# Kernel optimization log

Measured on AMD Instinct MI355X. Metric: run time of the kernel, lower is better.

Reference implementation:

```python
import jax, jax.numpy as jnp
import numpy as np
from jax import lax

T, IMG, C_IN = 2048, 84, 4
HID = 256
NUM_OUT = 18
FEAT = 6 * 6 * 32  # 84 -> 42 -> 21 -> 11 -> 6 with stride-2 SAME convs


def setup_inputs() -> dict:
    key = jax.random.key(0)
    ks = jax.random.split(key, 8)
    d = {}
    d["x"] = jax.random.normal(ks[0], (T, IMG, IMG, C_IN), jnp.float32)
    cin = C_IN
    for i in range(4):
        d[f"conv_w{i}"] = jax.random.normal(ks[1 + i], (3, 3, cin, 32), jnp.float32) * (1.0 / np.sqrt(9 * cin))
        d[f"conv_b{i}"] = jnp.zeros((32,), jnp.float32)
        cin = 32
    d["lstm_w"] = jax.random.normal(ks[5], (FEAT + HID, 4 * HID), jnp.float32) * (1.0 / np.sqrt(FEAT + HID))
    d["lstm_b"] = jnp.zeros((4 * HID,), jnp.float32)
    d["fc_w"] = jax.random.normal(ks[6], (HID, NUM_OUT), jnp.float32) * 0.01
    d["fc_b"] = jnp.zeros((NUM_OUT,), jnp.float32)
    d["c_in"] = jnp.zeros((1, HID), jnp.float32)
    d["h_in"] = jnp.zeros((1, HID), jnp.float32)
    return d


def _conv_stack(x, ws, bs):
    dn = ("NHWC", "HWIO", "NHWC")
    for w, b in zip(ws, bs):
        x = jax.nn.elu(lax.conv_general_dilated(x, w, (2, 2), "SAME", dimension_numbers=dn) + b)
    return x.reshape(x.shape[0], -1)  # [T, FEAT]


def _lstm(feats, c0, h0, lstm_w, lstm_b):
    # BasicLSTMCell: gates [i, j, f, o], forget_bias = 1.0
    def step(carry, xt):
        c, h = carry  # [1, HID] each
        z = jnp.concatenate([xt[None, :], h], axis=1) @ lstm_w + lstm_b
        i, j, f, o = jnp.split(z, 4, axis=1)
        c = c * jax.nn.sigmoid(f + 1.0) + jax.nn.sigmoid(i) * jnp.tanh(j)
        h = jnp.tanh(c) * jax.nn.sigmoid(o)
        return (c, h), h[0]

    (_, _), hs = lax.scan(step, (c0, h0), feats)
    return hs  # [T, HID]


def reference(x, c_in, h_in,
              conv_w0, conv_b0, conv_w1, conv_b1,
              conv_w2, conv_b2, conv_w3, conv_b3,
              lstm_w, lstm_b, fc_w, fc_b):
    feats = _conv_stack(x, [conv_w0, conv_w1, conv_w2, conv_w3],
                        [conv_b0, conv_b1, conv_b2, conv_b3])
    hs = _lstm(feats, c_in, h_in, lstm_w, lstm_b)
    logits = hs @ fc_w + fc_b  # [T, NUM_OUT]
    return logits, hs
```

## Files before the change

### kernel.cpp

```cpp
#include <hip/hip_runtime.h>
#include <hip/hip_bf16.h>

__device__ inline float fsig(float x) { return 1.0f / (1.0f + __expf(-x)); }
__device__ inline float ftanh(float x) {
    float ax = fabsf(x);
    float e = __expf(-2.0f * ax);
    float r = (1.0f - e) / (1.0f + e);
    return x >= 0.0f ? r : -r;
}
__device__ inline float felu(float x) { return x > 0.0f ? x : expm1f(x); }

typedef _Float16 h2_t __attribute__((ext_vector_type(2)));
typedef _Float16 f16x8 __attribute__((ext_vector_type(8)));
typedef float f32x4 __attribute__((ext_vector_type(4)));

__device__ inline unsigned int packh2(float a, float b) {
    unsigned short ua = __builtin_bit_cast(unsigned short, (_Float16)a);
    unsigned short ub = __builtin_bit_cast(unsigned short, (_Float16)b);
    return (unsigned int)ua | ((unsigned int)ub << 16);
}
__device__ inline unsigned short f16bits(float a) {
    return __builtin_bit_cast(unsigned short, (_Float16)a);
}

__device__ inline float dot2acc(unsigned int w, unsigned int h, float acc) {
#if __has_builtin(__builtin_amdgcn_fdot2)
    return __builtin_amdgcn_fdot2(__builtin_bit_cast(h2_t, w), __builtin_bit_cast(h2_t, h), acc, false);
#else
    _Float16 wlo = __builtin_bit_cast(_Float16, (unsigned short)(w & 0xffff));
    _Float16 whi = __builtin_bit_cast(_Float16, (unsigned short)(w >> 16));
    _Float16 hlo = __builtin_bit_cast(_Float16, (unsigned short)(h & 0xffff));
    _Float16 hhi = __builtin_bit_cast(_Float16, (unsigned short)(h >> 16));
    return acc + (float)wlo * (float)hlo + (float)whi * (float)hhi;
#endif
}

__global__ __launch_bounds__(256) void convert_lwT(const float* __restrict__ lw,
                                                   unsigned short* __restrict__ lwhT) {
    int idx = blockIdx.x * 256 + threadIdx.x;
    if (idx >= 1152 * 1024) return;
    int k = idx >> 10, n = idx & 1023;
    lwhT[(size_t)n * 1152 + k] = f16bits(lw[idx]);
}

__global__ __launch_bounds__(256) void conv0_kernel(const float* __restrict__ in,
                                                    const float* __restrict__ wg,
                                                    const float* __restrict__ bias,
                                                    unsigned short* __restrict__ out) {
    constexpr int W = 84, OW = 42, PAD = 0, WP = W + 2;
    __shared__ float in_s[3 * WP * 4];
    constexpr int NQ = 3 * WP;
    const int tid = threadIdx.x;
    const int oy = blockIdx.x;
    const int t = blockIdx.y;
    const int co = tid & 31;

    for (int q = tid; q < NQ; q += 256) {
        int ky = q / WP;
        int col = q - ky * WP;
        int iy = 2 * oy - PAD + ky;
        int ix = col - 1;
        float4 v = make_float4(0.f, 0.f, 0.f, 0.f);
        if (iy >= 0 && iy < W && ix >= 0 && ix < W)
            v = *(const float4*)&in[(((size_t)t * W + iy) * W + ix) * 4];
        *(float4*)&in_s[q * 4] = v;
    }

    float wr[9][4];
#pragma unroll
    for (int tap = 0; tap < 9; ++tap)
#pragma unroll
        for (int j = 0; j < 4; ++j) wr[tap][j] = wg[(tap * 4 + j) * 32 + co];
    __syncthreads();

    const int g = tid >> 5;
    constexpr int NOX = (OW + 7) / 8;
    float acc[NOX];
#pragma unroll
    for (int m = 0; m < NOX; ++m) acc[m] = 0.f;
#pragma unroll
    for (int ky = 0; ky < 3; ++ky)
#pragma unroll
        for (int kx = 0; kx < 3; ++kx) {
            float w0 = wr[ky * 3 + kx][0], w1 = wr[ky * 3 + kx][1];
            float w2 = wr[ky * 3 + kx][2], w3 = wr[ky * 3 + kx][3];
#pragma unroll
            for (int m = 0; m < NOX; ++m) {
                int ox = g + 8 * m;
                if (ox < OW) {
                    int cs = 2 * ox + kx - PAD + 1;
                    float4 xi = *(const float4*)&in_s[(ky * WP + cs) * 4];
                    acc[m] += xi.x * w0 + xi.y * w1 + xi.z * w2 + xi.w * w3;
                }
            }
        }
    float b = bias[co];
#pragma unroll
    for (int m = 0; m < NOX; ++m) {
        int ox = g + 8 * m;
        if (ox < OW)
            out[(((size_t)t * OW + oy) * OW + ox) * 32 + co] = f16bits(felu(acc[m] + b));
    }
}

template <int W, int OW, int PAD, bool F32OUT>
__global__ __launch_bounds__(256) void convh_kernel(const unsigned short* __restrict__ in,
                                                    const float* __restrict__ wg,
                                                    const float* __restrict__ bias,
                                                    void* __restrict__ outv) {
    constexpr int WP = W + 2;
    constexpr int OWQ = (OW + 3) / 4;
    __shared__ __align__(16) unsigned short in_s[3][WP][32];
    __shared__ float zs[4][OW * 32];

    const int tid = threadIdx.x;
    const int oy = blockIdx.x;
    const int t = blockIdx.y;
    const int co16 = tid & 15;
    const int cig = (tid >> 4) & 3;
    const int oxq = tid >> 6;

    constexpr int NQ4 = 3 * WP * 4;
    uint4* in_s4 = reinterpret_cast<uint4*>(&in_s[0][0][0]);
    for (int q = tid; q < NQ4; q += 256) {
        int ky = q / (WP * 4);
        int rem = q - ky * (WP * 4);
        int col = rem >> 2, c4 = rem & 3;
        int iy = 2 * oy - PAD + ky;
        int ix = col - 1;
        uint4 v = make_uint4(0u, 0u, 0u, 0u);
        if (iy >= 0 && iy < W && ix >= 0 && ix < W)
            v = *(const uint4*)&in[(((size_t)t * W + iy) * W + ix) * 32 + c4 * 8];
        in_s4[q] = v;
    }

    unsigned int wr[9][4][2];
#pragma unroll
    for (int tap = 0; tap < 9; ++tap)
#pragma unroll
        for (int p = 0; p < 4; ++p) {
            wr[tap][p][0] = packh2(wg[(tap * 32 + cig * 8 + 2 * p) * 32 + co16],
                                   wg[(tap * 32 + cig * 8 + 2 * p + 1) * 32 + co16]);
            wr[tap][p][1] = packh2(wg[(tap * 32 + cig * 8 + 2 * p) * 32 + co16 + 16],
                                   wg[(tap * 32 + cig * 8 + 2 * p + 1) * 32 + co16 + 16]);
        }
    __syncthreads();

    float acc0[OWQ], acc1[OWQ];
#pragma unroll
    for (int m = 0; m < OWQ; ++m) { acc0[m] = 0.f; acc1[m] = 0.f; }
#pragma unroll
    for (int ky = 0; ky < 3; ++ky)
#pragma unroll
        for (int kx = 0; kx < 3; ++kx) {
            const int tap = ky * 3 + kx;
#pragma unroll
            for (int m = 0; m < OWQ; ++m) {
                int ox = oxq * OWQ + m;
                if (ox < OW) {
                    int cs = 2 * ox + kx - PAD + 1;
                    uint4 h8 = *(const uint4*)&in_s[ky][cs][cig * 8];
                    acc0[m] = dot2acc(wr[tap][0][0], h8.x, acc0[m]);
                    acc0[m] = dot2acc(wr[tap][1][0], h8.y, acc0[m]);
                    acc0[m] = dot2acc(wr[tap][2][0], h8.z, acc0[m]);
                    acc0[m] = dot2acc(wr[tap][3][0], h8.w, acc0[m]);
                    acc1[m] = dot2acc(wr[tap][0][1], h8.x, acc1[m]);
                    acc1[m] = dot2acc(wr[tap][1][1], h8.y, acc1[m]);
                    acc1[m] = dot2acc(wr[tap][2][1], h8.z, acc1[m]);
                    acc1[m] = dot2acc(wr[tap][3][1], h8.w, acc1[m]);
                }
            }
        }
#pragma unroll
    for (int m = 0; m < OWQ; ++m) {
        int ox = oxq * OWQ + m;
        if (ox < OW) {
            zs[cig][ox * 32 + co16] = acc0[m];
            zs[cig][ox * 32 + co16 + 16] = acc1[m];
        }
    }
    __syncthreads();

    for (int idx = tid; idx < OW * 32; idx += 256) {
        float s = zs[0][idx] + zs[1][idx] + zs[2][idx] + zs[3][idx] + bias[idx & 31];
        s = felu(s);
        if constexpr (F32OUT)
            ((float*)outv)[(((size_t)t * OW + oy) * OW) * 32 + idx] = s;
        else
            ((unsigned short*)outv)[(((size_t)t * OW + oy) * OW) * 32 + idx] = f16bits(s);
    }
}

__global__ __launch_bounds__(256) void gemm_mfma(const unsigned short* __restrict__ A,
                                                 const unsigned short* __restrict__ BT,
                                                 const float* __restrict__ bias,
                                                 float* __restrict__ C) {
    __shared__ __align__(16) unsigned short As[64][40];
    __shared__ __align__(16) unsigned short Bs[64][40];
    const int bn = blockIdx.x;
    const int bm = blockIdx.y;
    const int tid = threadIdx.x;
    const int wv = tid >> 6;
    const int l = tid & 63;
    const int lm = l & 15;
    const int kg = l >> 4;

    f32x4 acc[4] = {};

    const int sr = tid >> 2;
    const int sk = (tid & 3) * 8;

    for (int k0 = 0; k0 < 1152; k0 += 32) {
        *(uint4*)&As[sr][sk] = *(const uint4*)&A[(size_t)(bm * 64 + sr) * 1152 + k0 + sk];
        *(uint4*)&Bs[sr][sk] = *(const uint4*)&BT[(size_t)(bn * 64 + sr) * 1152 + k0 + sk];
        __syncthreads();

        f16x8 a = *(const f16x8*)&As[(wv << 4) + lm][kg * 8];
        f16x8 b0 = *(const f16x8*)&Bs[lm][kg * 8];
        f16x8 b1 = *(const f16x8*)&Bs[16 + lm][kg * 8];
        f16x8 b2 = *(const f16x8*)&Bs[32 + lm][kg * 8];
        f16x8 b3 = *(const f16x8*)&Bs[48 + lm][kg * 8];
        acc[0] = __builtin_amdgcn_mfma_f32_16x16x32_f16(a, b0, acc[0], 0, 0, 0);
        acc[1] = __builtin_amdgcn_mfma_f32_16x16x32_f16(a, b1, acc[1], 0, 0, 0);
        acc[2] = __builtin_amdgcn_mfma_f32_16x16x32_f16(a, b2, acc[2], 0, 0, 0);
        acc[3] = __builtin_amdgcn_mfma_f32_16x16x32_f16(a, b3, acc[3], 0, 0, 0);
        __syncthreads();
    }

#pragma unroll
    for (int nt = 0; nt < 4; ++nt) {
        int col = bn * 64 + nt * 16 + lm;
        float bv = bias[col];
#pragma unroll
        for (int j = 0; j < 4; ++j) {
            int row = bm * 64 + (wv << 4) + kg * 4 + j;
            C[(size_t)row * 1024 + col] = acc[nt][j] + bv;
        }
    }
}

__global__ __attribute__((amdgpu_flat_work_group_size(512, 512)))
void lstm7_kernel(const float* __restrict__ lstm_w,
                  const float* __restrict__ xpart,
                  const float* __restrict__ c_in,
                  const float* __restrict__ h_in,
                  float* __restrict__ hs_out) {
    __shared__ __align__(16) unsigned int wl[512][52];
    __shared__ float zsm[2][4][256];
    __shared__ __align__(16) unsigned int hpk[2][2][68];

    const int tid = threadIdx.x;
    const int s = tid >> 8;
    const int u = tid & 255;

    for (int q = 0; q < 4; ++q)
        for (int p = 0; p < 12; ++p) {
            int gp = 64 * s + p;
            wl[tid][q * 12 + p] = packh2(lstm_w[(size_t)(1152 + 2 * gp) * 1024 + (q << 8) + u],
                                         lstm_w[(size_t)(1152 + 2 * gp + 1) * 1024 + (q << 8) + u]);
        }
    unsigned int wreg[4][52];
#pragma unroll
    for (int q = 0; q < 4; ++q)
        for (int p = 12; p < 64; ++p) {
            int gp = 64 * s + p;
            wreg[q][p - 12] = packh2(lstm_w[(size_t)(1152 + 2 * gp) * 1024 + (q << 8) + u],
                                     lstm_w[(size_t)(1152 + 2 * gp + 1) * 1024 + (q << 8) + u]);
        }

    float c_state = c_in[u];
    if (tid < 256) {
        unsigned short* hrow = (unsigned short*)&hpk[0][u >> 7][0];
        hrow[u & 127] = f16bits(h_in[u]);
    }
    __syncthreads();

    float xp0 = xpart[u], xp1 = xpart[256 + u], xp2 = xpart[512 + u], xp3 = xpart[768 + u];

    for (int t = 0; t < 2048; ++t) {
        const int cur = t & 1;
        const uint4* hq = reinterpret_cast<const uint4*>(&hpk[cur][s][0]);

        float a0 = 0.f, a1 = 0.f, a2 = 0.f, a3 = 0.f;
        {
            uint4 hA = hq[0], hB = hq[1], hC = hq[2];
            uint4 w0a = *(const uint4*)&wl[tid][0];
            uint4 w0b = *(const uint4*)&wl[tid][4];
            uint4 w0c = *(const uint4*)&wl[tid][8];
            a0 = dot2acc(w0a.x, hA.x, a0); a0 = dot2acc(w0a.y, hA.y, a0);
            a0 = dot2acc(w0a.z, hA.z, a0); a0 = dot2acc(w0a.w, hA.w, a0);
            a0 = dot2acc(w0b.x, hB.x, a0); a0 = dot2acc(w0b.y, hB.y, a0);
            a0 = dot2acc(w0b.z, hB.z, a0); a0 = dot2acc(w0b.w, hB.w, a0);
            a0 = dot2acc(w0c.x, hC.x, a0); a0 = dot2acc(w0c.y, hC.y, a0);
            a0 = dot2acc(w0c.z, hC.z, a0); a0 = dot2acc(w0c.w, hC.w, a0);
            uint4 w1a = *(const uint4*)&wl[tid][12];
            uint4 w1b = *(const uint4*)&wl[tid][16];
            uint4 w1c = *(const uint4*)&wl[tid][20];
            a1 = dot2acc(w1a.x, hA.x, a1); a1 = dot2acc(w1a.y, hA.y, a1);
            a1 = dot2acc(w1a.z, hA.z, a1); a1 = dot2acc(w1a.w, hA.w, a1);
            a1 = dot2acc(w1b.x, hB.x, a1); a1 = dot2acc(w1b.y, hB.y, a1);
            a1 = dot2acc(w1b.z, hB.z, a1); a1 = dot2acc(w1b.w, hB.w, a1);
            a1 = dot2acc(w1c.x, hC.x, a1); a1 = dot2acc(w1c.y, hC.y, a1);
            a1 = dot2acc(w1c.z, hC.z, a1); a1 = dot2acc(w1c.w, hC.w, a1);
            uint4 w2a = *(const uint4*)&wl[tid][24];
            uint4 w2b = *(const uint4*)&wl[tid][28];
            uint4 w2c = *(const uint4*)&wl[tid][32];
            a2 = dot2acc(w2a.x, hA.x, a2); a2 = dot2acc(w2a.y, hA.y, a2);
            a2 = dot2acc(w2a.z, hA.z, a2); a2 = dot2acc(w2a.w, hA.w, a2);
            a2 = dot2acc(w2b.x, hB.x, a2); a2 = dot2acc(w2b.y, hB.y, a2);
            a2 = dot2acc(w2b.z, hB.z, a2); a2 = dot2acc(w2b.w, hB.w, a2);
            a2 = dot2acc(w2c.x, hC.x, a2); a2 = dot2acc(w2c.y, hC.y, a2);
            a2 = dot2acc(w2c.z, hC.z, a2); a2 = dot2acc(w2c.w, hC.w, a2);
            uint4 w3a = *(const uint4*)&wl[tid][36];
            uint4 w3b = *(const uint4*)&wl[tid][40];
            uint4 w3c = *(const uint4*)&wl[tid][44];
            a3 = dot2acc(w3a.x, hA.x, a3); a3 = dot2acc(w3a.y, hA.y, a3);
            a3 = dot2acc(w3a.z, hA.z, a3); a3 = dot2acc(w3a.w, hA.w, a3);
            a3 = dot2acc(w3b.x, hB.x, a3); a3 = dot2acc(w3b.y, hB.y, a3);
            a3 = dot2acc(w3b.z, hB.z, a3); a3 = dot2acc(w3b.w, hB.w, a3);
            a3 = dot2acc(w3c.x, hC.x, a3); a3 = dot2acc(w3c.y, hC.y, a3);
            a3 = dot2acc(w3c.z, hC.z, a3); a3 = dot2acc(w3c.w, hC.w, a3);
        }
#pragma unroll
        for (int c = 3; c < 16; ++c) {
            uint4 h4 = hq[c];
            const int r = 4 * (c - 3);
            a0 = dot2acc(wreg[0][r + 0], h4.x, a0); a0 = dot2acc(wreg[0][r + 1], h4.y, a0);
            a0 = dot2acc(wreg[0][r + 2], h4.z, a0); a0 = dot2acc(wreg[0][r + 3], h4.w, a0);
            a1 = dot2acc(wreg[1][r + 0], h4.x, a1); a1 = dot2acc(wreg[1][r + 1], h4.y, a1);
            a1 = dot2acc(wreg[1][r + 2], h4.z, a1); a1 = dot2acc(wreg[1][r + 3], h4.w, a1);
            a2 = dot2acc(wreg[2][r + 0], h4.x, a2); a2 = dot2acc(wreg[2][r + 1], h4.y, a2);
            a2 = dot2acc(wreg[2][r + 2], h4.z, a2); a2 = dot2acc(wreg[2][r + 3], h4.w, a2);
            a3 = dot2acc(wreg[3][r + 0], h4.x, a3); a3 = dot2acc(wreg[3][r + 1], h4.y, a3);
            a3 = dot2acc(wreg[3][r + 2], h4.z, a3); a3 = dot2acc(wreg[3][r + 3], h4.w, a3);
        }
        zsm[s][0][u] = a0;
        zsm[s][1][u] = a1;
        zsm[s][2][u] = a2;
        zsm[s][3][u] = a3;

        float xn0 = 0.f, xn1 = 0.f, xn2 = 0.f, xn3 = 0.f;
        if (t + 1 < 2048) {
            const float* xr = &xpart[(size_t)(t + 1) * 1024];
            xn0 = xr[u]; xn1 = xr[256 + u]; xn2 = xr[512 + u]; xn3 = xr[768 + u];
        }

        asm volatile("s_waitcnt lgkmcnt(0)\n\ts_barrier" ::: "memory");

        float zi = zsm[0][0][u] + zsm[1][0][u] + xp0;
        float zj = zsm[0][1][u] + zsm[1][1][u] + xp1;
        float zf = zsm[0][2][u] + zsm[1][2][u] + xp2;
        float zo = zsm[0][3][u] + zsm[1][3][u] + xp3;
        c_state = c_state * fsig(zf + 1.0f) + fsig(zi) * ftanh(zj);
        float h = ftanh(c_state) * fsig(zo);
        if (tid < 256) {
            hs_out[(size_t)t * 256 + u] = h;
            unsigned short* hrow = (unsigned short*)&hpk[cur ^ 1][u >> 7][0];
            hrow[u & 127] = f16bits(h);
        }

        asm volatile("s_waitcnt lgkmcnt(0)\n\ts_barrier" ::: "memory");
        xp0 = xn0; xp1 = xn1; xp2 = xn2; xp3 = xn3;
    }
}

__global__ void logits_kernel(const float* __restrict__ hs, const float* __restrict__ fc_w,
                              const float* __restrict__ fc_b, float* __restrict__ out) {
    int idx = blockIdx.x * 256 + threadIdx.x;
    if (idx >= 2048 * 18) return;
    int t = idx / 18, n = idx % 18;
    float acc = fc_b[n];
    const float* hrow = hs + (size_t)t * 256;
#pragma unroll 4
    for (int k = 0; k < 256; ++k) acc += hrow[k] * fc_w[k * 18 + n];
    out[idx] = acc;
}

extern "C" void kernel_launch(void* const* d_in, const int* in_sizes, int n_in,
                              void* d_out, int out_size, void* d_ws, size_t ws_size,
                              hipStream_t stream) {
    const float* x   = (const float*)d_in[0];
    const float* w0  = (const float*)d_in[1];
    const float* b0  = (const float*)d_in[2];
    const float* w1  = (const float*)d_in[3];
    const float* b1  = (const float*)d_in[4];
    const float* w2  = (const float*)d_in[5];
    const float* b2  = (const float*)d_in[6];
    const float* w3  = (const float*)d_in[7];
    const float* b3  = (const float*)d_in[8];
    const float* lw  = (const float*)d_in[9];
    const float* lb  = (const float*)d_in[10];
    const float* fcw = (const float*)d_in[11];
    const float* fcb = (const float*)d_in[12];
    const float* cin = (const float*)d_in[13];
    const float* hin = (const float*)d_in[14];

    float* outp = (float*)d_out;
    float* hs_out = outp + 2048 * 18;

    float* xpart = (float*)d_ws;
    unsigned short* feats16 = (unsigned short*)(xpart + (size_t)2048 * 1024);
    unsigned short* lwhT = feats16 + (size_t)2048 * 1152;
    unsigned short* bufs = lwhT + (size_t)1024 * 1152;

    const size_t FIXED_B = (size_t)2048 * 1024 * 4 + (size_t)2048 * 1152 * 2 +
                           (size_t)1024 * 1152 * 2;
    const size_t PERT_B = ((size_t)56448 + 14112 + 3872) * 2;

    int C = 128;
    const int cands[5] = {2048, 1024, 512, 256, 128};
    for (int i = 0; i < 5; ++i) {
        if (FIXED_B + (size_t)cands[i] * PERT_B <= ws_size) { C = cands[i]; break; }
    }

    unsigned short* c0buf = bufs;
    unsigned short* c1buf = c0buf + (size_t)C * 56448;
    unsigned short* c2buf = c1buf + (size_t)C * 14112;

    convert_lwT<<<4608, 256, 0, stream>>>(lw, lwhT);

    for (int t0 = 0; t0 < 2048; t0 += C) {
        const float* xin = x + (size_t)t0 * 84 * 84 * 4;
        conv0_kernel<<<dim3(42, C), 256, 0, stream>>>(xin, w0, b0, c0buf);
        convh_kernel<42, 21, 0, false><<<dim3(21, C), 256, 0, stream>>>(c0buf, w1, b1, c1buf);
        convh_kernel<21, 11, 1, false><<<dim3(11, C), 256, 0, stream>>>(c1buf, w2, b2, c2buf);
        convh_kernel<11, 6, 1, false><<<dim3(6, C), 256, 0, stream>>>(
            c2buf, w3, b3, feats16 + (size_t)t0 * 1152);
    }

    gemm_mfma<<<dim3(16, 32), 256, 0, stream>>>(feats16, lwhT, lb, xpart);
    lstm7_kernel<<<1, 512, 0, stream>>>(lw, xpart, cin, hin, hs_out);
    logits_kernel<<<144, 256, 0, stream>>>(hs_out, fcw, fcb, outp);
}
```

Baseline: 4.377 ms.

## Broadcast LSTM hidden state via readlane and tile the weight transpose

The recurrent LSTM step now has each lane load one 16-byte slice of the packed hidden state and broadcasts it across the wavefront with readlane. This replaces per-lane LDS reads of the whole h vector and cuts LDS traffic on the serial critical path. Gate math and the xpart prefetch are restricted to the 256 threads that own outputs, removing redundant work in the second half of the block. The fp16 weight transpose becomes a shared-memory tiled transpose so both global reads and writes are coalesced. The readlane sequence adds scalar-unit instructions and may raise register pressure.

```diff
diff --git a/kernel.cpp b/kernel.cpp
--- a/kernel.cpp
+++ b/kernel.cpp
@@ -37,10 +37,15 @@
 
 __global__ __launch_bounds__(256) void convert_lwT(const float* __restrict__ lw,
                                                    unsigned short* __restrict__ lwhT) {
-    int idx = blockIdx.x * 256 + threadIdx.x;
-    if (idx >= 1152 * 1024) return;
-    int k = idx >> 10, n = idx & 1023;
-    lwhT[(size_t)n * 1152 + k] = f16bits(lw[idx]);
+    __shared__ float tile[32][33];
+    const int kb = blockIdx.x * 32;
+    const int nb = blockIdx.y * 32;
+    const int tx = threadIdx.x & 31, ty = threadIdx.x >> 5;
+    for (int i = ty; i < 32; i += 8)
+        tile[i][tx] = lw[(size_t)(kb + i) * 1024 + nb + tx];
+    __syncthreads();
+    for (int i = ty; i < 32; i += 8)
+        lwhT[(size_t)(nb + i) * 1152 + kb + tx] = f16bits(tile[tx][i]);
 }
 
 __global__ __launch_bounds__(256) void conv0_kernel(const float* __restrict__ in,
@@ -240,11 +245,11 @@
 }
 
 __global__ __attribute__((amdgpu_flat_work_group_size(512, 512)))
-void lstm7_kernel(const float* __restrict__ lstm_w,
-                  const float* __restrict__ xpart,
-                  const float* __restrict__ c_in,
-                  const float* __restrict__ h_in,
-                  float* __restrict__ hs_out) {
+void lstm10_kernel(const float* __restrict__ lstm_w,
+                   const float* __restrict__ xpart,
+                   const float* __restrict__ c_in,
+                   const float* __restrict__ h_in,
+                   float* __restrict__ hs_out) {
     __shared__ __align__(16) unsigned int wl[512][52];
     __shared__ float zsm[2][4][256];
     __shared__ __align__(16) unsigned int hpk[2][2][68];
@@ -275,64 +280,45 @@
     }
     __syncthreads();
 
-    float xp0 = xpart[u], xp1 = xpart[256 + u], xp2 = xpart[512 + u], xp3 = xpart[768 + u];
+    float xp0 = 0.f, xp1 = 0.f, xp2 = 0.f, xp3 = 0.f;
+    if (tid < 256) {
+        xp0 = xpart[u]; xp1 = xpart[256 + u]; xp2 = xpart[512 + u]; xp3 = xpart[768 + u];
+    }
 
     for (int t = 0; t < 2048; ++t) {
         const int cur = t & 1;
-        const uint4* hq = reinterpret_cast<const uint4*>(&hpk[cur][s][0]);
+        uint4 hv = *(const uint4*)&hpk[cur][s][(tid & 15) * 4];
+
+        unsigned int wlo[4][12];
+#pragma unroll
+        for (int q = 0; q < 4; ++q) {
+            *(uint4*)&wlo[q][0] = *(const uint4*)&wl[tid][q * 12 + 0];
+            *(uint4*)&wlo[q][4] = *(const uint4*)&wl[tid][q * 12 + 4];
+            *(uint4*)&wlo[q][8] = *(const uint4*)&wl[tid][q * 12 + 8];
+        }
 
         float a0 = 0.f, a1 = 0.f, a2 = 0.f, a3 = 0.f;
-        {
-            uint4 hA = hq[0], hB = hq[1], hC = hq[2];
-            uint4 w0a = *(const uint4*)&wl[tid][0];
-            uint4 w0b = *(const uint4*)&wl[tid][4];
-            uint4 w0c = *(const uint4*)&wl[tid][8];
-            a0 = dot2acc(w0a.x, hA.x, a0); a0 = dot2acc(w0a.y, hA.y, a0);
-            a0 = dot2acc(w0a.z, hA.z, a0); a0 = dot2acc(w0a.w, hA.w, a0);
-            a0 = dot2acc(w0b.x, hB.x, a0); a0 = dot2acc(w0b.y, hB.y, a0);
-            a0 = dot2acc(w0b.z, hB.z, a0); a0 = dot2acc(w0b.w, hB.w, a0);
-            a0 = dot2acc(w0c.x, hC.x, a0); a0 = dot2acc(w0c.y, hC.y, a0);
-            a0 = dot2acc(w0c.z, hC.z, a0); a0 = dot2acc(w0c.w, hC.w, a0);
-            uint4 w1a = *(const uint4*)&wl[tid][12];
-            uint4 w1b = *(const uint4*)&wl[tid][16];
-            uint4 w1c = *(const uint4*)&wl[tid][20];
-            a1 = dot2acc(w1a.x, hA.x, a1); a1 = dot2acc(w1a.y, hA.y, a1);
-            a1 = dot2acc(w1a.z, hA.z, a1); a1 = dot2acc(w1a.w, hA.w, a1);
-            a1 = dot2acc(w1b.x, hB.x, a1); a1 = dot2acc(w1b.y, hB.y, a1);
-            a1 = dot2acc(w1b.z, hB.z, a1); a1 = dot2acc(w1b.w, hB.w, a1);
-            a1 = dot2acc(w1c.x, hC.x, a1); a1 = dot2acc(w1c.y, hC.y, a1);
-            a1 = dot2acc(w1c.z, hC.z, a1); a1 = dot2acc(w1c.w, hC.w, a1);
-            uint4 w2a = *(const uint4*)&wl[tid][24];
-            uint4 w2b = *(const uint4*)&wl[tid][28];
-            uint4 w2c = *(const uint4*)&wl[tid][32];
-            a2 = dot2acc(w2a.x, hA.x, a2); a2 = dot2acc(w2a.y, hA.y, a2);
-            a2 = dot2acc(w2a.z, hA.z, a2); a2 = dot2acc(w2a.w, hA.w, a2);
-            a2 = dot2acc(w2b.x, hB.x, a2); a2 = dot2acc(w2b.y, hB.y, a2);
-            a2 = dot2acc(w2b.z, hB.z, a2); a2 = dot2acc(w2b.w, hB.w, a2);
-            a2 = dot2acc(w2c.x, hC.x, a2); a2 = dot2acc(w2c.y, hC.y, a2);
-            a2 = dot2acc(w2c.z, hC.z, a2); a2 = dot2acc(w2c.w, hC.w, a2);
-            uint4 w3a = *(const uint4*)&wl[tid][36];
-            uint4 w3b = *(const uint4*)&wl[tid][40];
-            uint4 w3c = *(const uint4*)&wl[tid][44];
-            a3 = dot2acc(w3a.x, hA.x, a3); a3 = dot2acc(w3a.y, hA.y, a3);
-            a3 = dot2acc(w3a.z, hA.z, a3); a3 = dot2acc(w3a.w, hA.w, a3);
-            a3 = dot2acc(w3b.x, hB.x, a3); a3 = dot2acc(w3b.y, hB.y, a3);
-            a3 = dot2acc(w3b.z, hB.z, a3); a3 = dot2acc(w3b.w, hB.w, a3);
-            a3 = dot2acc(w3c.x, hC.x, a3); a3 = dot2acc(w3c.y, hC.y, a3);
-            a3 = dot2acc(w3c.z, hC.z, a3); a3 = dot2acc(w3c.w, hC.w, a3);
-        }
-#pragma unroll
-        for (int c = 3; c < 16; ++c) {
-            uint4 h4 = hq[c];
-            const int r = 4 * (c - 3);
-            a0 = dot2acc(wreg[0][r + 0], h4.x, a0); a0 = dot2acc(wreg[0][r + 1], h4.y, a0);
-            a0 = dot2acc(wreg[0][r + 2], h4.z, a0); a0 = dot2acc(wreg[0][r + 3], h4.w, a0);
-            a1 = dot2acc(wreg[1][r + 0], h4.x, a1); a1 = dot2acc(wreg[1][r + 1], h4.y, a1);
-            a1 = dot2acc(wreg[1][r + 2], h4.z, a1); a1 = dot2acc(wreg[1][r + 3], h4.w, a1);
-            a2 = dot2acc(wreg[2][r + 0], h4.x, a2); a2 = dot2acc(wreg[2][r + 1], h4.y, a2);
-            a2 = dot2acc(wreg[2][r + 2], h4.z, a2); a2 = dot2acc(wreg[2][r + 3], h4.w, a2);
-            a3 = dot2acc(wreg[3][r + 0], h4.x, a3); a3 = dot2acc(wreg[3][r + 1], h4.y, a3);
-            a3 = dot2acc(wreg[3][r + 2], h4.z, a3); a3 = dot2acc(wreg[3][r + 3], h4.w, a3);
+#pragma unroll
+        for (int c = 0; c < 4; ++c) {
+            unsigned int hsg[16];
+#pragma unroll
+            for (int j = 0; j < 16; ++j) {
+                const int comp = j & 3;
+                unsigned int src = comp == 0 ? hv.x : comp == 1 ? hv.y : comp == 2 ? hv.z : hv.w;
+                hsg[j] = __builtin_amdgcn_readlane(src, 4 * c + (j >> 2));
+            }
+#pragma unroll
+            for (int j = 0; j < 16; ++j) {
+                const int p = c * 16 + j;
+                const unsigned int w0 = (p < 12) ? wlo[0][p < 12 ? p : 0] : wreg[0][p >= 12 ? p - 12 : 0];
+                const unsigned int w1 = (p < 12) ? wlo[1][p < 12 ? p : 0] : wreg[1][p >= 12 ? p - 12 : 0];
+                const unsigned int w2 = (p < 12) ? wlo[2][p < 12 ? p : 0] : wreg[2][p >= 12 ? p - 12 : 0];
+                const unsigned int w3 = (p < 12) ? wlo[3][p < 12 ? p : 0] : wreg[3][p >= 12 ? p - 12 : 0];
+                a0 = dot2acc(w0, hsg[j], a0);
+                a1 = dot2acc(w1, hsg[j], a1);
+                a2 = dot2acc(w2, hsg[j], a2);
+                a3 = dot2acc(w3, hsg[j], a3);
+            }
         }
         zsm[s][0][u] = a0;
         zsm[s][1][u] = a1;
@@ -340,20 +326,20 @@
         zsm[s][3][u] = a3;
 
         float xn0 = 0.f, xn1 = 0.f, xn2 = 0.f, xn3 = 0.f;
-        if (t + 1 < 2048) {
+        if (tid < 256 && t + 1 < 2048) {
             const float* xr = &xpart[(size_t)(t + 1) * 1024];
             xn0 = xr[u]; xn1 = xr[256 + u]; xn2 = xr[512 + u]; xn3 = xr[768 + u];
         }
 
         asm volatile("s_waitcnt lgkmcnt(0)\n\ts_barrier" ::: "memory");
 
-        float zi = zsm[0][0][u] + zsm[1][0][u] + xp0;
-        float zj = zsm[0][1][u] + zsm[1][1][u] + xp1;
-        float zf = zsm[0][2][u] + zsm[1][2][u] + xp2;
-        float zo = zsm[0][3][u] + zsm[1][3][u] + xp3;
-        c_state = c_state * fsig(zf + 1.0f) + fsig(zi) * ftanh(zj);
-        float h = ftanh(c_state) * fsig(zo);
         if (tid < 256) {
+            float zi = zsm[0][0][u] + zsm[1][0][u] + xp0;
+            float zj = zsm[0][1][u] + zsm[1][1][u] + xp1;
+            float zf = zsm[0][2][u] + zsm[1][2][u] + xp2;
+            float zo = zsm[0][3][u] + zsm[1][3][u] + xp3;
+            c_state = c_state * fsig(zf + 1.0f) + fsig(zi) * ftanh(zj);
+            float h = ftanh(c_state) * fsig(zo);
             hs_out[(size_t)t * 256 + u] = h;
             unsigned short* hrow = (unsigned short*)&hpk[cur ^ 1][u >> 7][0];
             hrow[u & 127] = f16bits(h);
@@ -417,7 +403,7 @@
     unsigned short* c1buf = c0buf + (size_t)C * 56448;
     unsigned short* c2buf = c1buf + (size_t)C * 14112;
 
-    convert_lwT<<<4608, 256, 0, stream>>>(lw, lwhT);
+    convert_lwT<<<dim3(36, 32), 256, 0, stream>>>(lw, lwhT);
 
     for (int t0 = 0; t0 < 2048; t0 += C) {
         const float* xin = x + (size_t)t0 * 84 * 84 * 4;
@@ -429,6 +415,6 @@
     }
 
     gemm_mfma<<<dim3(16, 32), 256, 0, stream>>>(feats16, lwhT, lb, xpart);
-    lstm7_kernel<<<1, 512, 0, stream>>>(lw, xpart, cin, hin, hs_out);
+    lstm10_kernel<<<1, 512, 0, stream>>>(lw, xpart, cin, hin, hs_out);
     logits_kernel<<<144, 256, 0, stream>>>(hs_out, fcw, fcb, outp);
 }
```

Measured after the change: 4.681 ms. 7.0% more time.
